# Kernel optimization log

Hardware: AMD Instinct MI355X
Metric: run time of the kernel (lower is better)

## Reference

```python
import jax, jax.numpy as jnp
import numpy as np

K = 7            # neighbor volumes (NNN heads)
PS = 10          # patch size
ADJ = PS // 2    # patch anchor offset (use_adj)
WOFF = 29 // 2   # search window half-size (ws=29)
KSEARCH = 224    # hardcoded in forward
T, C, E, HH, WW = 1, 8, 8, 64, 64


def _box1(a, axis):
    # sliding-window sum of length PS anchored at i-ADJ, zero outside
    pw = [(0, 0)] * a.ndim
    pw[axis] = (ADJ, PS - 1 - ADJ)
    ap = jnp.pad(a, pw)
    c = jnp.cumsum(ap, axis=axis)
    zp = [(0, 0)] * a.ndim
    zp[axis] = (1, 0)
    c = jnp.pad(c, zp)
    n = a.shape[axis]
    return jax.lax.slice_in_dim(c, PS, PS + n, axis=axis) - jax.lax.slice_in_dim(c, 0, n, axis=axis)


def box_sum(a):
    return _box1(_box1(a, -2), -1)


def setup_inputs():
    key = jax.random.key(0)
    ks = jax.random.split(key, 5)
    x = jax.random.normal(ks[0], (T, C, HH, WW), jnp.float32)
    xe = jax.random.normal(ks[1], (T, E, HH, WW), jnp.float32)
    ye = jax.random.normal(ks[2], (T, E, HH, WW), jnp.float32)
    y = jax.random.normal(ks[3], (T, C, HH, WW), jnp.float32)
    log_temp = 0.1 * jax.random.normal(ks[4], (T, 1, HH, WW), jnp.float32)
    return {"x": x, "xe": xe, "ye": ye, "y": y, "log_temp": log_temp}


def reference(x, xe, ye, y, log_temp):
    pad = lambda a: jnp.pad(a, ((0, 0), (0, 0), (1, 1), (1, 1)))
    x, xe, ye, y, log_temp = pad(x), pad(xe), pad(ye), pad(y), pad(log_temp)
    H, W = x.shape[-2:]
    Q = H * W
    xe0, ye0 = xe[0], ye[0]
    # search window offsets (ws x ws)
    dy, dx = np.meshgrid(np.arange(-WOFF, WOFF + 1), np.arange(-WOFF, WOFF + 1), indexing='ij')
    dy = jnp.asarray(dy.ravel()); dx = jnp.asarray(dx.ravel())
    nW = dy.shape[0]  # 841
    # patch squared norms (zero padded patches)
    n2_q = box_sum((ye0 ** 2).sum(0))   # (H,W)
    n2_db = box_sum((xe0 ** 2).sum(0))  # (H,W)
    xep = jnp.pad(xe0, ((0, 0), (WOFF, WOFF), (WOFF, WOFF)))
    n2p = jnp.pad(n2_db, WOFF)
    def shifted(d):
        s = jax.lax.dynamic_slice(xep, (0, WOFF + d[0], WOFF + d[1]), (E, H, W))
        n = jax.lax.dynamic_slice(n2p, (WOFF + d[0], WOFF + d[1]), (H, W))
        return s, n
    xe_s, n2_s = jax.vmap(shifted)(jnp.stack([dy, dx], -1))  # (nW,E,H,W),(nW,H,W)
    cross = box_sum((ye0[None] * xe_s).sum(1))               # (nW,H,W)
    dist = n2_q[None] + n2_s - 2.0 * cross                   # L2^2, (nW,H,W)
    qy = jnp.arange(H)[:, None]; qx = jnp.arange(W)[None, :]
    valid = ((qy[None] + dy[:, None, None] >= 0) & (qy[None] + dy[:, None, None] < H)
             & (qx[None] + dx[:, None, None] >= 0) & (qx[None] + dx[:, None, None] < W))
    self_m = (dy == 0) & (dx == 0)  # remove_self
    dist = jnp.where(valid & ~self_m[:, None, None], dist, 1e10)
    dist = dist.transpose(1, 2, 0).reshape(Q, nW)
    negd, idx = jax.lax.top_k(-dist, KSEARCH)  # closest KSEARCH, negd = -L2
    # avg-pooled log temperature per query patch
    lt = (box_sum(log_temp[0, 0]) / (PS * PS)).reshape(Q)
    # NeuralNearestNeighbors: iterative continuous top-k relaxation
    logits = negd / jnp.exp(lt)[:, None]
    Ws = []
    for _ in range(K):
        w = jax.nn.softmax(logits, axis=-1)
        logits = logits + jnp.log(jnp.clip(1.0 - w, 1e-6, None))
        Ws.append(w)
    Wk = jnp.stack(Ws)  # (K,Q,KSEARCH)
    # absolute candidate coords
    qyf = jnp.repeat(jnp.arange(H), W); qxf = jnp.tile(jnp.arange(W), H)
    ny = qyf[:, None] + dy[idx]; nx = qxf[:, None] + dx[idx]  # (Q,KSEARCH)
    # weighted patch sum (gather per patch offset)
    xpad = jnp.pad(x[0], ((0, 0), (ADJ, PS - 1 - ADJ), (ADJ, PS - 1 - ADJ)))
    z = jnp.zeros((K, Q, C, PS, PS), x.dtype)
    for oy in range(PS):
        for ox in range(PS):
            vals = xpad[:, ny + oy, nx + ox]  # (C,Q,KSEARCH)
            z = z.at[:, :, :, oy, ox].set(jnp.einsum('kqj,cqj->kqc', Wk, vals))
    # fold with counting (iFoldz): overlap-add of patches + coverage counts
    zp = z.transpose(1, 0, 2, 3, 4).reshape(H, W, K * C, PS, PS)
    buf = jnp.zeros((K * C, H + PS - 1, W + PS - 1), x.dtype)
    cnt = jnp.zeros((H + PS - 1, W + PS - 1), x.dtype)
    for oy in range(PS):
        for ox in range(PS):
            buf = buf.at[:, oy:oy + H, ox:ox + W].add(zp[:, :, :, oy, ox].transpose(2, 0, 1))
            cnt = cnt.at[oy:oy + H, ox:ox + W].add(1.0)
    vid = buf[:, ADJ:ADJ + H, ADJ:ADJ + W]
    zvid = cnt[ADJ:ADJ + H, ADJ:ADJ + W]
    zagg = vid / zvid[None]
    zagg = zagg.reshape(T, K, C, H, W) - y.reshape(T, 1, C, H, W)
    zagg = zagg.reshape(T, K * C, H, W)
    out = jnp.concatenate([y, zagg], axis=1)[..., 1:-1, 1:-1]
    return out
```

## Files before the change

### kernel.cpp

```cpp
#include <hip/hip_runtime.h>
#include <hip/hip_bf16.h>

#define HP    66
#define QTOT  (HP*HP)
#define NWIN  29
#define NW    (NWIN*NWIN)
#define KK    7
#define WOFF2 14
#define NZ    15
#define QB    8
#define QBN   545
#define NIT   27
#define NSEG3 198
#define PSTR  4368


__global__ __launch_bounds__(256) void k_prep1(const float* __restrict__ x,
    const float* __restrict__ xe, const float* __restrict__ ye,
    const float* __restrict__ lt, float* __restrict__ ws) {
  int p = blockIdx.x * 256 + threadIdx.x;
  if (p >= QTOT) return;
  int i = p / HP, j = p % HP;
  bool in = (i >= 1 && i < HP-1 && j >= 1 && j < HP-1);
  int src = (i-1)*64 + (j-1);
  float vy[8], vx[8], vv[8];
  float sy = 0.f, sx = 0.f;
#pragma unroll
  for (int e = 0; e < 8; ++e) {
    vy[e] = in ? ye[e*4096 + src] : 0.f;
    vx[e] = in ? xe[e*4096 + src] : 0.f;
    vv[e] = in ? x [e*4096 + src] : 0.f;
    sy += vy[e]*vy[e]; sx += vx[e]*vx[e];
  }
  float4* yp = (float4*)(ws + (size_t)p*8);
  float4* xp = (float4*)(ws + 8*QTOT + (size_t)p*8);
  float4* vp = (float4*)(ws + 16*QTOT + (size_t)p*8);
  yp[0] = make_float4(vy[0], vy[1], vy[2], vy[3]);
  yp[1] = make_float4(vy[4], vy[5], vy[6], vy[7]);
  xp[0] = make_float4(vx[0], vx[1], vx[2], vx[3]);
  xp[1] = make_float4(vx[4], vx[5], vx[6], vx[7]);
  vp[0] = make_float4(vv[0], vv[1], vv[2], vv[3]);
  vp[1] = make_float4(vv[4], vv[5], vv[6], vv[7]);
  ws[24*QTOT + p] = sy;
  ws[25*QTOT + p] = sx;
  ws[26*QTOT + p] = in ? lt[src] : 0.f;
}

__global__ __launch_bounds__(256) void k_prep2(float* __restrict__ ws) {
  int p = blockIdx.x * 256 + threadIdx.x;
  if (p >= QTOT) return;
  int i = p / HP, j = p % HP;
  const float* sqye = ws + 24*QTOT;
  const float* sqxe = ws + 25*QTOT;
  const float* lt66 = ws + 26*QTOT;
  float a = 0.f, b = 0.f, c = 0.f;
  for (int u = -5; u <= 4; ++u) {
    int ii = i + u; if (ii < 0 || ii >= HP) continue;
    for (int v = -5; v <= 4; ++v) {
      int jj = j + v; if (jj < 0 || jj >= HP) continue;
      int o = ii*HP + jj;
      a += sqye[o]; b += sqxe[o]; c += lt66[o];
    }
  }
  ws[27*QTOT + p] = a;
  ws[28*QTOT + p] = b;
  ws[29*QTOT + p] = c * 0.01f;
}

__global__ __launch_bounds__(256) void k_dist(const float* __restrict__ ws,
                                              float* __restrict__ dist) {
  __shared__ float4 s4[QTOT/4];
  __shared__ float h[QTOT];
  float* s = (float*)s4;
  int w = blockIdx.x, tid = threadIdx.x;
  int dy = w / NWIN - WOFF2, dx = w % NWIN - WOFF2;
  const float* yex = ws;
  const float* xex = ws + 8*QTOT;
  const float* n2q  = ws + 27*QTOT;
  const float* n2db = ws + 28*QTOT;
  for (int p = tid; p < QTOT; p += 256) {
    int i = p / HP, j = p % HP;
    int ii = i + dy, jj = j + dx;
    float sv = 0.f;
    if (ii >= 0 && ii < HP && jj >= 0 && jj < HP) {
      int p2 = ii*HP + jj;
      const float4* yp = (const float4*)(yex + (size_t)p*8);
      const float4* xp = (const float4*)(xex + (size_t)p2*8);
      float4 a0 = yp[0], a1 = yp[1], b0 = xp[0], b1 = xp[1];
      sv += a0.x*b0.x; sv += a0.y*b0.y; sv += a0.z*b0.z; sv += a0.w*b0.w;
      sv += a1.x*b1.x; sv += a1.y*b1.y; sv += a1.z*b1.z; sv += a1.w*b1.w;
    }
    s[p] = sv;
  }
  __syncthreads();
  if (tid < NSEG3) {
    int row = tid % HP, seg = tid / HP, c0 = seg*22;
    const float* ar = s + row*HP;
    float* hr = h + row*HP;
    float w9[9]; float sum = 0.f;
#pragma unroll
    for (int t = 0; t < 9; ++t) {
      int jj = c0 - 5 + t;
      float v = (jj >= 0) ? ar[jj] : 0.f;
      w9[t] = v; sum += v;
    }
#pragma unroll
    for (int t = 0; t < 22; ++t) {
      int j = c0 + t, jn = j + 4;
      float nv = (jn < HP) ? ar[jn] : 0.f;
      sum += nv;
      hr[j] = sum;
      sum -= w9[t % 9];
      w9[t % 9] = nv;
    }
  }
  __syncthreads();
  if (tid < NSEG3) {
    int col = tid % HP, seg = tid / HP, r0 = seg*22;
    float w9[9]; float sum = 0.f;
#pragma unroll
    for (int t = 0; t < 9; ++t) {
      int ii = r0 - 5 + t;
      float v = (ii >= 0) ? h[ii*HP + col] : 0.f;
      w9[t] = v; sum += v;
    }
#pragma unroll
    for (int t = 0; t < 22; ++t) {
      int i = r0 + t, in2 = i + 4;
      float nv = (in2 < HP) ? h[in2*HP + col] : 0.f;
      sum += nv;
      float cr = sum;
      int p = i*HP + col;
      int ii = i + dy, jj = col + dx;
      bool valid = (ii >= 0 && ii < HP && jj >= 0 && jj < HP);
      float dv = 1e10f;
      if (valid && !(dy == 0 && dx == 0))
        dv = n2q[p] + n2db[ii*HP + jj] - 2.f * cr;
      s[p] = dv;
      sum -= w9[t % 9];
      w9[t % 9] = nv;
    }
  }
  __syncthreads();
  float4* dq = (float4*)(dist + (size_t)w*QTOT);
  for (int p4 = tid; p4 < QTOT/4; p4 += 256)
    dq[p4] = s4[p4];
}

__global__ __launch_bounds__(256) void k_weights(const float* __restrict__ ws,
    const float* __restrict__ dist, __hip_bfloat16* __restrict__ wf) {
  __shared__ float mh[32], sh[32];
  int tid = threadIdx.x;
  int qq = tid & (QB-1);
  int qb = blockIdx.x;
  int q = qb * QB + qq;
  bool qok = q < QTOT;
  int qs = qok ? q : (QTOT - 1);
  int wg = tid >> 3;
  int wave = tid >> 6;
  float invT = __expf(-ws[29*QTOT + qs]);
  float lv[NIT];
#pragma unroll
  for (int it = 0; it < NIT; ++it) {
    int w = wg + it*32;
    lv[it] = (qok && w < NW) ? (-dist[w*QTOT + qs] * invT) : -3.0e38f;
  }
  for (int k = 0; k < KK; ++k) {
    float pm = -3.0e38f;
#pragma unroll
    for (int it = 0; it < NIT; ++it) pm = fmaxf(pm, lv[it]);
    pm = fmaxf(pm, __shfl_xor(pm, 8, 64));
    pm = fmaxf(pm, __shfl_xor(pm, 16, 64));
    pm = fmaxf(pm, __shfl_xor(pm, 32, 64));
    if ((tid & 63) < QB) mh[wave*QB + qq] = pm;
    __syncthreads();
    float m = fmaxf(fmaxf(mh[qq], mh[QB+qq]), fmaxf(mh[2*QB+qq], mh[3*QB+qq]));
    float psum = 0.f;
#pragma unroll
    for (int it = 0; it < NIT; ++it) psum += __expf(lv[it] - m);
    psum += __shfl_xor(psum, 8, 64);
    psum += __shfl_xor(psum, 16, 64);
    psum += __shfl_xor(psum, 32, 64);
    if ((tid & 63) < QB) sh[wave*QB + qq] = psum;
    __syncthreads();
    float invden = 1.0f / (sh[qq] + sh[QB+qq] + sh[2*QB+qq] + sh[3*QB+qq]);
    size_t bkq = ((size_t)k*QBN + qb)*NW;
#pragma unroll
    for (int it = 0; it < NIT; ++it) {
      int w = wg + it*32;
      if (qok && w < NW) {
        float wgt = __expf(lv[it] - m) * invden;
        wf[(bkq + w)*8 + qq] = __float2bfloat16(wgt);
        if (k < KK-1 && wgt > 1e-9f)
          lv[it] += __logf(fmaxf(1.f - wgt, 1e-6f));
      }
    }
    __syncthreads();
  }
}

__global__ __launch_bounds__(256) void k_boxw(const __hip_bfloat16* __restrict__ wfa,
                                              __hip_bfloat16* __restrict__ wfb) {
  __shared__ uint4 au4[546];
  __shared__ uint4 hu4[546];
  int bid = blockIdx.x;
  int l = (bid & 7)*736 + (bid >> 3);
  if (l >= KK*NW) return;
  int k = l / NW, w = l % NW;
  const uint4* u4 = (const uint4*)wfa;
  size_t pb = ((size_t)k*QBN)*NW + w;
  int tid = threadIdx.x;
  for (int qb = tid; qb < QBN; qb += 256)
    au4[qb] = u4[pb + (size_t)qb*NW];
  if (tid < 12) ((unsigned short*)au4)[4356 + tid] = 0;
  __syncthreads();
  const unsigned short* a16 = (const unsigned short*)au4;
  unsigned short* h16 = (unsigned short*)hu4;
  for (int task = tid; task < 396; task += 256) {
    int row = task % HP, seg = task / HP, c0 = seg*11;
    const unsigned short* ar = a16 + row*HP;
    unsigned short* hr = h16 + row*HP;
    float w9[9]; float sum = 0.f;
#pragma unroll
    for (int t = 0; t < 9; ++t) {
      int jj = c0 - 4 + t;
      float v = (jj >= 0) ? __uint_as_float((unsigned)ar[jj] << 16) : 0.f;
      w9[t] = v; sum += v;
    }
#pragma unroll
    for (int t = 0; t < 11; ++t) {
      int j = c0 + t, jn = j + 5;
      float nv = (jn < HP) ? __uint_as_float((unsigned)ar[jn] << 16) : 0.f;
      sum += nv;
      hr[j] = __bfloat16_as_ushort(__float2bfloat16(sum));
      sum -= w9[t % 9];
      w9[t % 9] = nv;
    }
  }
  __syncthreads();
  unsigned short* a16w = (unsigned short*)au4;
  for (int task = tid; task < 396; task += 256) {
    int col = task % HP, seg = task / HP, r0 = seg*11;
    float w9[9]; float sum = 0.f;
#pragma unroll
    for (int t = 0; t < 9; ++t) {
      int ii = r0 - 4 + t;
      float v = (ii >= 0) ? __uint_as_float((unsigned)h16[ii*HP + col] << 16) : 0.f;
      w9[t] = v; sum += v;
    }
#pragma unroll
    for (int t = 0; t < 11; ++t) {
      int i = r0 + t, in2 = i + 5;
      float nv = (in2 < HP) ? __uint_as_float((unsigned)h16[in2*HP + col] << 16) : 0.f;
      sum += nv;
      a16w[i*HP + col] = __bfloat16_as_ushort(__float2bfloat16(sum));
      sum -= w9[t % 9];
      w9[t % 9] = nv;
    }
  }
  __syncthreads();
  uint4* out4 = (uint4*)(wfb + ((size_t)k*NW + w)*PSTR);
  for (int qb = tid; qb < 546; qb += 256)
    out4[qb] = au4[qb];
}

__global__ __launch_bounds__(256) void k_contract(const float* __restrict__ ws,
    const unsigned short* __restrict__ wfb, float* __restrict__ accb2) {
  __shared__ float xt[17][44][8];
  int t = blockIdx.x, z = blockIdx.y, k = blockIdx.z, tid = threadIdx.x;
  int I0 = (t >> 2) * 16, J0 = (t & 3) * 16;
  int dylo = -WOFF2 + 2*z;
  int gy0 = I0 + 1 + dylo, gx0 = J0 - 13;
  const float* x66i = ws + 16*QTOT;
  for (int idx = tid; idx < 17*44; idx += 256) {
    int r = idx / 44, cc = idx % 44;
    int gy = gy0 + r, gx = gx0 + cc;
    float4 v0 = make_float4(0.f,0.f,0.f,0.f), v1 = v0;
    if (gy >= 0 && gy < HP && gx >= 0 && gx < HP) {
      const float4* xp = (const float4*)(x66i + (size_t)(gy*HP + gx)*8);
      v0 = xp[0]; v1 = xp[1];
    }
    float4* d = (float4*)&xt[r][cc][0];
    d[0] = v0; d[1] = v1;
  }
  __syncthreads();
  int il = tid >> 4, jl = tid & 15;
  int I = I0 + 1 + il, J = J0 + 1 + jl;
  int pix = I*HP + J;
  float acc[8];
#pragma unroll
  for (int c = 0; c < 8; ++c) acc[c] = 0.f;
  int ndd = (z == NZ-1) ? 1 : 2;
  for (int dd = 0; dd < ndd; ++dd) {
    int wrow = (dylo + dd + WOFF2) * NWIN;
    const unsigned short* wp = wfb + ((size_t)k*NW + wrow)*PSTR + pix;
    unsigned short wv[NWIN];
#pragma unroll
    for (int dxw = 0; dxw < NWIN; ++dxw) wv[dxw] = wp[(size_t)dxw*PSTR];
    int r = il + dd;
#pragma unroll
    for (int dxw = 0; dxw < NWIN; ++dxw) {
      float wgt = __uint_as_float((unsigned)wv[dxw] << 16);
      const float4* xr = (const float4*)&xt[r][jl + dxw][0];
      float4 x0 = xr[0], x1 = xr[1];
      acc[0] += wgt * x0.x; acc[1] += wgt * x0.y;
      acc[2] += wgt * x0.z; acc[3] += wgt * x0.w;
      acc[4] += wgt * x1.x; acc[5] += wgt * x1.y;
      acc[6] += wgt * x1.z; acc[7] += wgt * x1.w;
    }
  }
  int px64 = (I-1)*64 + (J-1);
#pragma unroll
  for (int c = 0; c < 8; ++c)
    accb2[((z*56 + k*8 + c)*4096) + px64] = acc[c];
}

__global__ __launch_bounds__(256) void k_final(const float* __restrict__ y,
    const float* __restrict__ accb2, float* __restrict__ out) {
  int idx = blockIdx.x * 256 + threadIdx.x;
  int ch = idx >> 12, px = idx & 4095;
  if (ch < 8) { out[idx] = y[ch*4096 + px]; return; }
  int kc = ch - 8, c = kc & 7;
  int i = px >> 6, j = px & 63;
  int I = i + 1, J = j + 1;
  int cy = min(I+5, HP-1) - max(I-4, 0) + 1;
  int cx = min(J+5, HP-1) - max(J-4, 0) + 1;
  float s = 0.f;
  for (int z = 0; z < NZ; ++z) s += accb2[(z*56 + kc)*4096 + px];
  out[idx] = s / (float)(cy*cx) - y[c*4096 + px];
}

extern "C" void kernel_launch(void* const* d_in, const int* in_sizes, int n_in,
                              void* d_out, int out_size, void* d_ws, size_t ws_size,
                              hipStream_t stream) {
  const float* x  = (const float*)d_in[0];
  const float* xe = (const float*)d_in[1];
  const float* ye = (const float*)d_in[2];
  const float* y  = (const float*)d_in[3];
  const float* lt = (const float*)d_in[4];
  float* ws   = (float*)d_ws;
  float* dist = ws + 30*QTOT;
  __hip_bfloat16* wfa = (__hip_bfloat16*)(dist + (size_t)NW*QTOT);
  __hip_bfloat16* wfb = wfa + (size_t)KK*QBN*NW*8;
  float* accb2 = dist;
  float* out = (float*)d_out;

  k_prep1<<<(QTOT + 255)/256, 256, 0, stream>>>(x, xe, ye, lt, ws);
  k_prep2<<<(QTOT + 255)/256, 256, 0, stream>>>(ws);
  k_dist<<<NW, 256, 0, stream>>>(ws, dist);
  k_weights<<<QBN, 256, 0, stream>>>(ws, dist, wfa);
  k_boxw<<<KK*NW, 256, 0, stream>>>(wfa, wfb);
  k_contract<<<dim3(16, NZ, KK), 256, 0, stream>>>(ws, (const unsigned short*)wfb, accb2);
  k_final<<<out_size/256, 256, 0, stream>>>(y, accb2, out);
}
```

Baseline: 145.3 us.

## Write softmax weights directly in plane layout and box-filter them in place

k_weights now stores each bf16 weight straight into the per-(k,w) plane layout that k_contract consumes, instead of an intermediate blocked-by-query layout. k_boxw then loads and stores its plane contiguously in place, so the strided 16-byte gather and the second weight buffer are gone. The k_weights block index is also remapped so each XCD handles a contiguous range of query blocks, which may improve L2 locality on the dist reads. One risk: the padding tail of each plane is no longer explicitly zeroed.

```diff
diff --git a/kernel.cpp b/kernel.cpp
--- a/kernel.cpp
+++ b/kernel.cpp
@@ -151,8 +151,10 @@
     const float* __restrict__ dist, __hip_bfloat16* __restrict__ wf) {
   __shared__ float mh[32], sh[32];
   int tid = threadIdx.x;
+  int bid = blockIdx.x;
+  int xcd = bid & 7, idx = bid >> 3;
+  int qb = (xcd == 0) ? idx : (69 + (xcd-1)*68 + idx);
   int qq = tid & (QB-1);
-  int qb = blockIdx.x;
   int q = qb * QB + qq;
   bool qok = q < QTOT;
   int qs = qok ? q : (QTOT - 1);
@@ -184,13 +186,13 @@
     if ((tid & 63) < QB) sh[wave*QB + qq] = psum;
     __syncthreads();
     float invden = 1.0f / (sh[qq] + sh[QB+qq] + sh[2*QB+qq] + sh[3*QB+qq]);
-    size_t bkq = ((size_t)k*QBN + qb)*NW;
+    size_t kbase = (size_t)k*NW*PSTR + q;
 #pragma unroll
     for (int it = 0; it < NIT; ++it) {
       int w = wg + it*32;
       if (qok && w < NW) {
         float wgt = __expf(lv[it] - m) * invden;
-        wf[(bkq + w)*8 + qq] = __float2bfloat16(wgt);
+        wf[kbase + (size_t)w*PSTR] = __float2bfloat16(wgt);
         if (k < KK-1 && wgt > 1e-9f)
           lv[it] += __logf(fmaxf(1.f - wgt, 1e-6f));
       }
@@ -199,20 +201,14 @@
   }
 }
 
-__global__ __launch_bounds__(256) void k_boxw(const __hip_bfloat16* __restrict__ wfa,
-                                              __hip_bfloat16* __restrict__ wfb) {
+__global__ __launch_bounds__(256) void k_boxw(__hip_bfloat16* __restrict__ wfp) {
   __shared__ uint4 au4[546];
   __shared__ uint4 hu4[546];
   int bid = blockIdx.x;
-  int l = (bid & 7)*736 + (bid >> 3);
-  if (l >= KK*NW) return;
-  int k = l / NW, w = l % NW;
-  const uint4* u4 = (const uint4*)wfa;
-  size_t pb = ((size_t)k*QBN)*NW + w;
+  uint4* plane = (uint4*)(wfp + (size_t)bid*PSTR);
   int tid = threadIdx.x;
-  for (int qb = tid; qb < QBN; qb += 256)
-    au4[qb] = u4[pb + (size_t)qb*NW];
-  if (tid < 12) ((unsigned short*)au4)[4356 + tid] = 0;
+  for (int qb = tid; qb < 546; qb += 256)
+    au4[qb] = plane[qb];
   __syncthreads();
   const unsigned short* a16 = (const unsigned short*)au4;
   unsigned short* h16 = (unsigned short*)hu4;
@@ -259,9 +255,8 @@
     }
   }
   __syncthreads();
-  uint4* out4 = (uint4*)(wfb + ((size_t)k*NW + w)*PSTR);
   for (int qb = tid; qb < 546; qb += 256)
-    out4[qb] = au4[qb];
+    plane[qb] = au4[qb];
 }
 
 __global__ __launch_bounds__(256) void k_contract(const float* __restrict__ ws,
@@ -340,16 +335,15 @@
   const float* lt = (const float*)d_in[4];
   float* ws   = (float*)d_ws;
   float* dist = ws + 30*QTOT;
-  __hip_bfloat16* wfa = (__hip_bfloat16*)(dist + (size_t)NW*QTOT);
-  __hip_bfloat16* wfb = wfa + (size_t)KK*QBN*NW*8;
+  __hip_bfloat16* wf = (__hip_bfloat16*)(dist + (size_t)NW*QTOT);
   float* accb2 = dist;
   float* out = (float*)d_out;
 
   k_prep1<<<(QTOT + 255)/256, 256, 0, stream>>>(x, xe, ye, lt, ws);
   k_prep2<<<(QTOT + 255)/256, 256, 0, stream>>>(ws);
   k_dist<<<NW, 256, 0, stream>>>(ws, dist);
-  k_weights<<<QBN, 256, 0, stream>>>(ws, dist, wfa);
-  k_boxw<<<KK*NW, 256, 0, stream>>>(wfa, wfb);
-  k_contract<<<dim3(16, NZ, KK), 256, 0, stream>>>(ws, (const unsigned short*)wfb, accb2);
+  k_weights<<<QBN, 256, 0, stream>>>(ws, dist, wf);
+  k_boxw<<<KK*NW, 256, 0, stream>>>(wf);
+  k_contract<<<dim3(16, NZ, KK), 256, 0, stream>>>(ws, (const unsigned short*)wf, accb2);
   k_final<<<out_size/256, 256, 0, stream>>>(y, accb2, out);
 }
```

Result: no change. 144.4 us (-0.7%).
